# Kernel tuning notes

Hardware: AMD Instinct MI355X
Metric: run time of the kernel (lower is better)

The kernel has to match this reference:

```python
import jax, jax.numpy as jnp
import numpy as np

N_NODES = 100000
N_EDGES = 640000
D_IN = 128
D_OUT = 128


def setup_inputs() -> dict:
    key = jax.random.key(0)
    k_x, k_w, k_v, k_r, k_c = jax.random.split(key, 5)
    x = jax.random.normal(k_x, (N_NODES, D_IN), dtype=jnp.float32)
    # Xavier-uniform init for weights, zeros for bias (matches module init)
    limit = float(np.sqrt(6.0 / (D_IN + D_OUT)))
    weights = jax.random.uniform(k_w, (D_IN, D_OUT), dtype=jnp.float32,
                                 minval=-limit, maxval=limit)
    bias = jnp.zeros((D_OUT,), dtype=jnp.float32)
    # Sparse normalized adjacency in COO form: value[e] * y[col[e]] scattered to row[e]
    edge_val = jax.random.uniform(k_v, (N_EDGES,), dtype=jnp.float32)
    row = jax.random.randint(k_r, (N_EDGES,), 0, N_NODES, dtype=jnp.int32)
    col = jax.random.randint(k_c, (N_EDGES,), 0, N_NODES, dtype=jnp.int32)
    return {"x": x, "weights": weights, "bias": bias,
            "edge_val": edge_val, "row": row, "col": col}


def reference(x, weights, bias, edge_val, row, col):
    # y = x @ W  (dense GEMM)  [N, D_OUT]
    y = x @ weights
    # SpMM: out[i] = sum_{e: row[e]==i} edge_val[e] * y[col[e]]
    msg = edge_val[:, None] * y[col]            # [E, D_OUT] irregular gather
    agg = jax.ops.segment_sum(msg, row, num_segments=x.shape[0])
    return agg + bias
```

## Files before the change

### kernel.cpp

```cpp
#include <hip/hip_runtime.h>
#include <hip/hip_bf16.h>


#define N_NODES 100000
#define N_EDGES 640000
#define D 128
#define ELL_K 16
#define OVF_CAP 8192
#define NB 391
#define BCAP 2048
#define CHUNK 2048
#define NCHUNKS 313
#define N_TILES 6250
#define ELL_P 17

typedef __attribute__((ext_vector_type(8))) short short8;
typedef __attribute__((ext_vector_type(4))) float f32x4;
typedef __attribute__((ext_vector_type(4))) ushort us4;

__device__ __forceinline__ ushort f2bf(float f) {
    uint u = __float_as_uint(f);
    u += 0x7fff + ((u >> 16) & 1);
    return (ushort)(u >> 16);
}
__device__ __forceinline__ float bflo(uint u) { return __uint_as_float(u << 16); }
__device__ __forceinline__ float bfhi(uint u) { return __uint_as_float(u & 0xffff0000u); }

__global__ __launch_bounds__(256, 4) void gemm_xw(const float* __restrict__ x,
                                                  const float* __restrict__ w,
                                                  ushort* __restrict__ y,
                                                  int* __restrict__ bucketCnt) {
    __shared__ ushort wt[128 * 128];
    const int tid = threadIdx.x;

    int gz = blockIdx.x * 256 + tid;
    if (gz <= NB) bucketCnt[gz] = 0;

    #pragma unroll
    for (int it = 0; it < 16; ++it) {
        int idx4 = tid + it * 256;
        int k = idx4 >> 5;
        int n0 = (idx4 & 31) * 4;
        float4 v = *(const float4*)(w + (size_t)idx4 * 4);
        float vv[4] = {v.x, v.y, v.z, v.w};
        #pragma unroll
        for (int q = 0; q < 4; ++q) {
            int n = n0 + q;
            wt[n * 128 + (k ^ ((n & 7) << 3))] = f2bf(vv[q]);
        }
    }
    __syncthreads();

    const int lane = tid & 63;
    const int l15 = lane & 15;
    const int h = lane >> 4;

    const int waveGlobal = blockIdx.x * 4 + (tid >> 6);
    const int nWaves = gridDim.x * 4;

    for (int t = waveGlobal; t < N_TILES; t += nWaves) {
        asm volatile("" ::: "memory");
        const float* xr = x + (size_t)(t * 16 + l15) * D;
        float4 xb[8];
        #pragma unroll
        for (int ks = 0; ks < 4; ++ks) {
            xb[2 * ks]     = *(const float4*)(xr + 32 * ks + 8 * h);
            xb[2 * ks + 1] = *(const float4*)(xr + 32 * ks + 8 * h + 4);
        }
        short8 a[4];
        #pragma unroll
        for (int ks = 0; ks < 4; ++ks) {
            const float* p0 = (const float*)&xb[2 * ks];
            const float* p1 = (const float*)&xb[2 * ks + 1];
            a[ks][0] = f2bf(p0[0]); a[ks][1] = f2bf(p0[1]);
            a[ks][2] = f2bf(p0[2]); a[ks][3] = f2bf(p0[3]);
            a[ks][4] = f2bf(p1[0]); a[ks][5] = f2bf(p1[1]);
            a[ks][6] = f2bf(p1[2]); a[ks][7] = f2bf(p1[3]);
        }
        f32x4 acc[8];
        #pragma unroll
        for (int j = 0; j < 8; ++j) acc[j] = (f32x4){0.f, 0.f, 0.f, 0.f};
        #pragma unroll
        for (int ks = 0; ks < 4; ++ks) {
            const int k0 = 32 * ks + 8 * h;
            #pragma unroll
            for (int j = 0; j < 8; ++j) {
                int n = 16 * j + l15;
                short8 b = *(const short8*)&wt[n * 128 + (k0 ^ ((n & 7) << 3))];
                acc[j] = __builtin_amdgcn_mfma_f32_16x16x32_bf16(b, a[ks], acc[j], 0, 0, 0);
            }
        }
        ushort* yn = y + (size_t)(t * 16 + l15) * D;
        #pragma unroll
        for (int j = 0; j < 8; ++j) {
            us4 o;
            o.x = f2bf(acc[j][0]); o.y = f2bf(acc[j][1]);
            o.z = f2bf(acc[j][2]); o.w = f2bf(acc[j][3]);
            *(us4*)(yn + 16 * j + 4 * h) = o;
        }
    }
}

__global__ __launch_bounds__(256) void partition_edges(const float* __restrict__ ev,
                                                       const int* __restrict__ row,
                                                       const int* __restrict__ col,
                                                       int* __restrict__ bucketCnt,
                                                       uint2* __restrict__ es0,
                                                       int* __restrict__ ovfCnt,
                                                       int* __restrict__ ovfRow,
                                                       int* __restrict__ ovfCol,
                                                       float* __restrict__ ovfVal) {
    __shared__ int hist[NB];
    __shared__ int cur[NB];
    const int tid = threadIdx.x;
    const int base = blockIdx.x * CHUNK;

    for (int t = tid; t < NB; t += 256) hist[t] = 0;
    __syncthreads();

    #pragma unroll
    for (int it = 0; it < CHUNK / 256; ++it) {
        int i = base + it * 256 + tid;
        if (i < N_EDGES) atomicAdd(&hist[row[i] >> 8], 1);
    }
    __syncthreads();

    for (int t = tid; t < NB; t += 256) {
        int h = hist[t];
        int start = (h > 0) ? atomicAdd(&bucketCnt[t], h) : 0;
        cur[t] = t * BCAP + start;
    }
    __syncthreads();

    #pragma unroll
    for (int it = 0; it < CHUNK / 256; ++it) {
        int i = base + it * 256 + tid;
        if (i < N_EDGES) {
            int r = row[i];
            int b = r >> 8;
            int p = atomicAdd(&cur[b], 1);
            if (p < (b + 1) * BCAP) {
                uint2 e;
                e.x = __float_as_uint(ev[i]);
                e.y = (uint)col[i] | ((uint)(r & 255) << 20);
                es0[p] = e;
            } else {
                int q = atomicAdd(ovfCnt, 1);
                if (q < OVF_CAP) {
                    ovfRow[q] = r;
                    ovfCol[q] = col[i];
                    ovfVal[q] = ev[i];
                }
            }
        }
    }
}

__global__ __launch_bounds__(256) void build_ell(const uint2* __restrict__ es0,
                                                 const int* __restrict__ bucketCnt,
                                                 float2* __restrict__ es,
                                                 int* __restrict__ ovfCnt,
                                                 int* __restrict__ ovfRow,
                                                 int* __restrict__ ovfCol,
                                                 float* __restrict__ ovfVal) {
    __shared__ float2 ell[256 * ELL_P];
    __shared__ int lcnt[256];
    const int tid = threadIdx.x;
    const int b = blockIdx.x;

    lcnt[tid] = 0;
    #pragma unroll
    for (int it = 0; it < ELL_P; ++it)
        ell[it * 256 + tid] = (float2){0.f, 0.f};
    __syncthreads();

    int cnt = bucketCnt[b];
    if (cnt > BCAP) cnt = BCAP;
    const uint2* src = es0 + (size_t)b * BCAP;

    for (int i = tid; i < cnt; i += 256) {
        uint2 e = src[i];
        int r = e.y >> 20;
        int p = atomicAdd(&lcnt[r], 1);
        if (p < ELL_K) {
            float2 rec;
            rec.x = __uint_as_float(e.x);
            rec.y = __uint_as_float(e.y & 0xFFFFFu);
            ell[r * ELL_P + p] = rec;
        } else {
            int q = atomicAdd(ovfCnt, 1);
            if (q < OVF_CAP) {
                ovfRow[q] = b * 256 + r;
                ovfCol[q] = (int)(e.y & 0xFFFFFu);
                ovfVal[q] = __uint_as_float(e.x);
            }
        }
    }
    __syncthreads();

    const int nbase = b * 256;
    int nvalid = N_NODES - nbase;
    if (nvalid > 256) nvalid = 256;

    float2* dst2 = es + (size_t)nbase * ELL_K;
    for (int t = tid; t < nvalid * ELL_K; t += 256) {
        int r = t >> 4, s = t & 15;
        dst2[t] = ell[r * ELL_P + s];
    }
}

__global__ __launch_bounds__(256) void spmm_ell(const ushort* __restrict__ y,
                                                const float2* __restrict__ es,
                                                const float* __restrict__ bias,
                                                float* __restrict__ out) {
    const int tid = threadIdx.x;
    const int c16 = tid & 15;
    const int n = blockIdx.x * 16 + (tid >> 4);

    const float4* er = (const float4*)(es + (size_t)n * ELL_K);
    float4 e0 = er[0], e1 = er[1], e2 = er[2], e3 = er[3];
    float4 e4 = er[4], e5 = er[5], e6 = er[6], e7 = er[7];

    const ushort* yb = y + c16 * 8;
    #define YLD(c) (*(const uint4*)(yb + ((size_t)__float_as_int(c) << 7)))
    uint4 u0 = YLD(e0.y), u1 = YLD(e0.w), u2 = YLD(e1.y), u3 = YLD(e1.w);
    uint4 u4 = YLD(e2.y), u5 = YLD(e2.w), u6 = YLD(e3.y), u7 = YLD(e3.w);
    uint4 u8 = YLD(e4.y), u9 = YLD(e4.w), uA = YLD(e5.y), uB = YLD(e5.w);
    uint4 uC = YLD(e6.y), uD = YLD(e6.w), uE = YLD(e7.y), uF = YLD(e7.w);
    #undef YLD

    float a[8] = {0.f, 0.f, 0.f, 0.f, 0.f, 0.f, 0.f, 0.f};
    #define FMA8(v, u) do { \
        a[0] += (v) * bflo((u).x); a[1] += (v) * bfhi((u).x); \
        a[2] += (v) * bflo((u).y); a[3] += (v) * bfhi((u).y); \
        a[4] += (v) * bflo((u).z); a[5] += (v) * bfhi((u).z); \
        a[6] += (v) * bflo((u).w); a[7] += (v) * bfhi((u).w); } while (0)
    FMA8(e0.x, u0); FMA8(e0.z, u1); FMA8(e1.x, u2); FMA8(e1.z, u3);
    FMA8(e2.x, u4); FMA8(e2.z, u5); FMA8(e3.x, u6); FMA8(e3.z, u7);
    FMA8(e4.x, u8); FMA8(e4.z, u9); FMA8(e5.x, uA); FMA8(e5.z, uB);
    FMA8(e6.x, uC); FMA8(e6.z, uD); FMA8(e7.x, uE); FMA8(e7.z, uF);
    #undef FMA8

    const float4 b0 = *(const float4*)(bias + c16 * 8);
    const float4 b1 = *(const float4*)(bias + c16 * 8 + 4);
    float4 o0 = {a[0] + b0.x, a[1] + b0.y, a[2] + b0.z, a[3] + b0.w};
    float4 o1 = {a[4] + b1.x, a[5] + b1.y, a[6] + b1.z, a[7] + b1.w};
    float* orow = out + ((size_t)n << 7) + c16 * 8;
    *(float4*)orow = o0;
    *(float4*)(orow + 4) = o1;
}

__global__ void ovf_fix(const ushort* __restrict__ y, const int* __restrict__ ovfRow,
                        const int* __restrict__ ovfCol, const float* __restrict__ ovfVal,
                        const int* __restrict__ ovfCnt, float* __restrict__ out) {
    int nOvf = *ovfCnt;
    if (nOvf > OVF_CAP) nOvf = OVF_CAP;
    int total = nOvf * 32;
    for (int idx = blockIdx.x * 256 + threadIdx.x; idx < total; idx += gridDim.x * 256) {
        int e = idx >> 5;
        int c = idx & 31;
        int r = ovfRow[e];
        int col = ovfCol[e];
        float v = ovfVal[e];
        uint2 u = *(const uint2*)(y + ((size_t)col << 7) + c * 4);
        atomicAdd(&out[(size_t)r * D + c * 4 + 0], v * bflo(u.x));
        atomicAdd(&out[(size_t)r * D + c * 4 + 1], v * bfhi(u.x));
        atomicAdd(&out[(size_t)r * D + c * 4 + 2], v * bflo(u.y));
        atomicAdd(&out[(size_t)r * D + c * 4 + 3], v * bfhi(u.y));
    }
}

extern "C" void kernel_launch(void* const* d_in, const int* in_sizes, int n_in,
                              void* d_out, int out_size, void* d_ws, size_t ws_size,
                              hipStream_t stream) {
    const float* x = (const float*)d_in[0];
    const float* w = (const float*)d_in[1];
    const float* bias = (const float*)d_in[2];
    const float* ev = (const float*)d_in[3];
    const int* row = (const int*)d_in[4];
    const int* col = (const int*)d_in[5];
    float* out = (float*)d_out;

    size_t off = 0;
    auto carve = [&](size_t bytes) -> void* {
        void* p = (char*)d_ws + off;
        off += (bytes + 255) & ~(size_t)255;
        return p;
    };
    ushort* y = (ushort*)carve((size_t)N_NODES * D * sizeof(ushort));
    float2* es = (float2*)carve((size_t)N_NODES * ELL_K * sizeof(float2));
    uint2* es0 = (uint2*)carve((size_t)NB * BCAP * sizeof(uint2));
    int* bucketCnt = (int*)carve((NB + 1) * sizeof(int));
    int* ovfCnt = bucketCnt + NB;
    int* ovfRow = (int*)carve(OVF_CAP * sizeof(int));
    int* ovfCol = (int*)carve(OVF_CAP * sizeof(int));
    float* ovfVal = (float*)carve(OVF_CAP * sizeof(float));

    gemm_xw<<<782, 256, 0, stream>>>(x, w, y, bucketCnt);
    partition_edges<<<NCHUNKS, 256, 0, stream>>>(ev, row, col, bucketCnt, es0,
                                                 ovfCnt, ovfRow, ovfCol, ovfVal);
    build_ell<<<NB, 256, 0, stream>>>(es0, bucketCnt, es,
                                      ovfCnt, ovfRow, ovfCol, ovfVal);
    spmm_ell<<<N_NODES / 16, 256, 0, stream>>>(y, es, bias, out);
    ovf_fix<<<16, 256, 0, stream>>>(y, ovfRow, ovfCol, ovfVal, ovfCnt, out);
}
```

Baseline: 88.21 us.

## Fuse ELL build into SpMM kernel with four row-slices per bucket

```diff
diff --git a/kernel.cpp b/kernel.cpp
--- a/kernel.cpp
+++ b/kernel.cpp
@@ -9,10 +9,11 @@
 #define OVF_CAP 8192
 #define NB 391
 #define BCAP 2048
-#define CHUNK 2048
-#define NCHUNKS 313
+#define CHUNK 4096
+#define NCHUNKS 157
 #define N_TILES 6250
-#define ELL_P 17
+#define ELL_P 18
+#define NSLICE 1564
 
 typedef __attribute__((ext_vector_type(8))) short short8;
 typedef __attribute__((ext_vector_type(4))) float f32x4;
@@ -156,22 +157,27 @@
     }
 }
 
-__global__ __launch_bounds__(256) void build_ell(const uint2* __restrict__ es0,
-                                                 const int* __restrict__ bucketCnt,
-                                                 float2* __restrict__ es,
-                                                 int* __restrict__ ovfCnt,
-                                                 int* __restrict__ ovfRow,
-                                                 int* __restrict__ ovfCol,
-                                                 float* __restrict__ ovfVal) {
-    __shared__ float2 ell[256 * ELL_P];
-    __shared__ int lcnt[256];
+__global__ __launch_bounds__(256) void ell_spmm(const uint2* __restrict__ es0,
+                                                const int* __restrict__ bucketCnt,
+                                                const ushort* __restrict__ y,
+                                                const float* __restrict__ bias,
+                                                float* __restrict__ out,
+                                                int* __restrict__ ovfCnt,
+                                                int* __restrict__ ovfRow,
+                                                int* __restrict__ ovfCol,
+                                                float* __restrict__ ovfVal) {
+    __shared__ float2 ell[64 * ELL_P];
+    __shared__ int lcnt[64];
     const int tid = threadIdx.x;
-    const int b = blockIdx.x;
-
-    lcnt[tid] = 0;
+    const int b = blockIdx.x >> 2;
+    const int slice = blockIdx.x & 3;
+
+    if (tid < 64) lcnt[tid] = 0;
     #pragma unroll
-    for (int it = 0; it < ELL_P; ++it)
-        ell[it * 256 + tid] = (float2){0.f, 0.f};
+    for (int it = 0; it < (64 * ELL_P + 255) / 256; ++it) {
+        int t = it * 256 + tid;
+        if (t < 64 * ELL_P) ell[t] = (float2){0.f, 0.f};
+    }
     __syncthreads();
 
     int cnt = bucketCnt[b];
@@ -181,73 +187,69 @@
     for (int i = tid; i < cnt; i += 256) {
         uint2 e = src[i];
         int r = e.y >> 20;
-        int p = atomicAdd(&lcnt[r], 1);
-        if (p < ELL_K) {
-            float2 rec;
-            rec.x = __uint_as_float(e.x);
-            rec.y = __uint_as_float(e.y & 0xFFFFFu);
-            ell[r * ELL_P + p] = rec;
-        } else {
-            int q = atomicAdd(ovfCnt, 1);
-            if (q < OVF_CAP) {
-                ovfRow[q] = b * 256 + r;
-                ovfCol[q] = (int)(e.y & 0xFFFFFu);
-                ovfVal[q] = __uint_as_float(e.x);
+        if ((r >> 6) == slice) {
+            int rl = r & 63;
+            int p = atomicAdd(&lcnt[rl], 1);
+            if (p < ELL_K) {
+                float2 rec;
+                rec.x = __uint_as_float(e.x);
+                rec.y = __uint_as_float(e.y & 0xFFFFFu);
+                ell[rl * ELL_P + p] = rec;
+            } else {
+                int q = atomicAdd(ovfCnt, 1);
+                if (q < OVF_CAP) {
+                    ovfRow[q] = b * 256 + r;
+                    ovfCol[q] = (int)(e.y & 0xFFFFFu);
+                    ovfVal[q] = __uint_as_float(e.x);
+                }
             }
         }
     }
     __syncthreads();
 
-    const int nbase = b * 256;
-    int nvalid = N_NODES - nbase;
-    if (nvalid > 256) nvalid = 256;
-
-    float2* dst2 = es + (size_t)nbase * ELL_K;
-    for (int t = tid; t < nvalid * ELL_K; t += 256) {
-        int r = t >> 4, s = t & 15;
-        dst2[t] = ell[r * ELL_P + s];
-    }
-}
-
-__global__ __launch_bounds__(256) void spmm_ell(const ushort* __restrict__ y,
-                                                const float2* __restrict__ es,
-                                                const float* __restrict__ bias,
-                                                float* __restrict__ out) {
-    const int tid = threadIdx.x;
     const int c16 = tid & 15;
-    const int n = blockIdx.x * 16 + (tid >> 4);
-
-    const float4* er = (const float4*)(es + (size_t)n * ELL_K);
-    float4 e0 = er[0], e1 = er[1], e2 = er[2], e3 = er[3];
-    float4 e4 = er[4], e5 = er[5], e6 = er[6], e7 = er[7];
-
-    const ushort* yb = y + c16 * 8;
-    #define YLD(c) (*(const uint4*)(yb + ((size_t)__float_as_int(c) << 7)))
-    uint4 u0 = YLD(e0.y), u1 = YLD(e0.w), u2 = YLD(e1.y), u3 = YLD(e1.w);
-    uint4 u4 = YLD(e2.y), u5 = YLD(e2.w), u6 = YLD(e3.y), u7 = YLD(e3.w);
-    uint4 u8 = YLD(e4.y), u9 = YLD(e4.w), uA = YLD(e5.y), uB = YLD(e5.w);
-    uint4 uC = YLD(e6.y), uD = YLD(e6.w), uE = YLD(e7.y), uF = YLD(e7.w);
-    #undef YLD
-
-    float a[8] = {0.f, 0.f, 0.f, 0.f, 0.f, 0.f, 0.f, 0.f};
-    #define FMA8(v, u) do { \
-        a[0] += (v) * bflo((u).x); a[1] += (v) * bfhi((u).x); \
-        a[2] += (v) * bflo((u).y); a[3] += (v) * bfhi((u).y); \
-        a[4] += (v) * bflo((u).z); a[5] += (v) * bfhi((u).z); \
-        a[6] += (v) * bflo((u).w); a[7] += (v) * bfhi((u).w); } while (0)
-    FMA8(e0.x, u0); FMA8(e0.z, u1); FMA8(e1.x, u2); FMA8(e1.z, u3);
-    FMA8(e2.x, u4); FMA8(e2.z, u5); FMA8(e3.x, u6); FMA8(e3.z, u7);
-    FMA8(e4.x, u8); FMA8(e4.z, u9); FMA8(e5.x, uA); FMA8(e5.z, uB);
-    FMA8(e6.x, uC); FMA8(e6.z, uD); FMA8(e7.x, uE); FMA8(e7.z, uF);
-    #undef FMA8
+    const int grp = tid >> 4;
+    const int nbase = blockIdx.x * 64;
 
     const float4 b0 = *(const float4*)(bias + c16 * 8);
     const float4 b1 = *(const float4*)(bias + c16 * 8 + 4);
-    float4 o0 = {a[0] + b0.x, a[1] + b0.y, a[2] + b0.z, a[3] + b0.w};
-    float4 o1 = {a[4] + b1.x, a[5] + b1.y, a[6] + b1.z, a[7] + b1.w};
-    float* orow = out + ((size_t)n << 7) + c16 * 8;
-    *(float4*)orow = o0;
-    *(float4*)(orow + 4) = o1;
+    const ushort* yb = y + c16 * 8;
+
+    #pragma unroll 1
+    for (int rep = 0; rep < 4; ++rep) {
+        const int rl = grp * 4 + rep;
+        const int n = nbase + rl;
+        const float4* er = (const float4*)&ell[rl * ELL_P];
+        float4 e0 = er[0], e1 = er[1], e2 = er[2], e3 = er[3];
+        float4 e4 = er[4], e5 = er[5], e6 = er[6], e7 = er[7];
+
+        #define YLD(c) (*(const uint4*)(yb + ((size_t)__float_as_int(c) << 7)))
+        uint4 u0 = YLD(e0.y), u1 = YLD(e0.w), u2 = YLD(e1.y), u3 = YLD(e1.w);
+        uint4 u4 = YLD(e2.y), u5 = YLD(e2.w), u6 = YLD(e3.y), u7 = YLD(e3.w);
+        uint4 u8 = YLD(e4.y), u9 = YLD(e4.w), uA = YLD(e5.y), uB = YLD(e5.w);
+        uint4 uC = YLD(e6.y), uD = YLD(e6.w), uE = YLD(e7.y), uF = YLD(e7.w);
+        #undef YLD
+
+        float a[8] = {0.f, 0.f, 0.f, 0.f, 0.f, 0.f, 0.f, 0.f};
+        #define FMA8(v, u) do { \
+            a[0] += (v) * bflo((u).x); a[1] += (v) * bfhi((u).x); \
+            a[2] += (v) * bflo((u).y); a[3] += (v) * bfhi((u).y); \
+            a[4] += (v) * bflo((u).z); a[5] += (v) * bfhi((u).z); \
+            a[6] += (v) * bflo((u).w); a[7] += (v) * bfhi((u).w); } while (0)
+        FMA8(e0.x, u0); FMA8(e0.z, u1); FMA8(e1.x, u2); FMA8(e1.z, u3);
+        FMA8(e2.x, u4); FMA8(e2.z, u5); FMA8(e3.x, u6); FMA8(e3.z, u7);
+        FMA8(e4.x, u8); FMA8(e4.z, u9); FMA8(e5.x, uA); FMA8(e5.z, uB);
+        FMA8(e6.x, uC); FMA8(e6.z, uD); FMA8(e7.x, uE); FMA8(e7.z, uF);
+        #undef FMA8
+
+        if (n < N_NODES) {
+            float4 o0 = {a[0] + b0.x, a[1] + b0.y, a[2] + b0.z, a[3] + b0.w};
+            float4 o1 = {a[4] + b1.x, a[5] + b1.y, a[6] + b1.z, a[7] + b1.w};
+            float* orow = out + ((size_t)n << 7) + c16 * 8;
+            *(float4*)orow = o0;
+            *(float4*)(orow + 4) = o1;
+        }
+    }
 }
 
 __global__ void ovf_fix(const ushort* __restrict__ y, const int* __restrict__ ovfRow,
@@ -288,7 +290,6 @@
         return p;
     };
     ushort* y = (ushort*)carve((size_t)N_NODES * D * sizeof(ushort));
-    float2* es = (float2*)carve((size_t)N_NODES * ELL_K * sizeof(float2));
     uint2* es0 = (uint2*)carve((size_t)NB * BCAP * sizeof(uint2));
     int* bucketCnt = (int*)carve((NB + 1) * sizeof(int));
     int* ovfCnt = bucketCnt + NB;
@@ -299,8 +300,7 @@
     gemm_xw<<<782, 256, 0, stream>>>(x, w, y, bucketCnt);
     partition_edges<<<NCHUNKS, 256, 0, stream>>>(ev, row, col, bucketCnt, es0,
                                                  ovfCnt, ovfRow, ovfCol, ovfVal);
-    build_ell<<<NB, 256, 0, stream>>>(es0, bucketCnt, es,
-                                      ovfCnt, ovfRow, ovfCol, ovfVal);
-    spmm_ell<<<N_NODES / 16, 256, 0, stream>>>(y, es, bias, out);
+    ell_spmm<<<NSLICE, 256, 0, stream>>>(es0, bucketCnt, y, bias, out,
+                                         ovfCnt, ovfRow, ovfCol, ovfVal);
     ovf_fix<<<16, 256, 0, stream>>>(y, ovfRow, ovfCol, ovfVal, ovfCnt, out);
 }
```

After: 87.34 us. No clear change (-1.0%).
